# Kernel optimization log

Hardware: AMD Instinct MI355X
Metric: run time of the kernel (lower is better)

The kernel has to match this reference:

```python
import jax, jax.numpy as jnp
import numpy as np

D_IN = 768
D_OUT = 768
NUM_HEADS = 12
HEAD_DIM = D_OUT // NUM_HEADS


def setup_inputs() -> dict:
    key = jax.random.key(0)
    ks = jax.random.split(key, 6)
    s = 0.02
    x = jax.random.normal(ks[0], (2, 4096, D_IN), dtype=jnp.float32)
    w_query = jax.random.normal(ks[1], (D_IN, D_OUT), dtype=jnp.float32) * s
    w_key = jax.random.normal(ks[2], (D_IN, D_OUT), dtype=jnp.float32) * s
    w_value = jax.random.normal(ks[3], (D_IN, D_OUT), dtype=jnp.float32) * s
    w_out = jax.random.normal(ks[4], (D_OUT, D_OUT), dtype=jnp.float32) * s
    b_out = jnp.zeros((D_OUT,), dtype=jnp.float32)
    return {"x": x, "w_query": w_query, "w_key": w_key, "w_value": w_value,
            "w_out": w_out, "b_out": b_out}


def reference(x, w_query, w_key, w_value, w_out, b_out):
    b, n, _ = x.shape
    # projections -> [b, n, h, d]
    q = (x @ w_query).reshape(b, n, NUM_HEADS, HEAD_DIM)
    k = (x @ w_key).reshape(b, n, NUM_HEADS, HEAD_DIM)
    v = (x @ w_value).reshape(b, n, NUM_HEADS, HEAD_DIM)
    # scores [b, h, q, k]
    scores = jnp.einsum('bqhd,bkhd->bhqk', q, k)
    causal = jnp.triu(jnp.ones((n, n), dtype=bool), k=1)  # True above diagonal
    scores = jnp.where(causal, -jnp.inf, scores)
    scale = 1.0 / jnp.sqrt(jnp.asarray(HEAD_DIM, dtype=scores.dtype))
    weights = jax.nn.softmax(scores * scale, axis=-1)
    # dropout p=0.0 -> identity
    ctx = jnp.einsum('bhqk,bkhd->bqhd', weights, v).reshape(b, n, D_OUT)
    return ctx @ w_out + b_out
```

## Files before the change

kernel.cpp:

```cpp
#include <hip/hip_runtime.h>

typedef unsigned short ushort_t;
typedef __bf16 bf16_t;
typedef float floatx4 __attribute__((ext_vector_type(4)));
typedef bf16_t bf16x8 __attribute__((ext_vector_type(8)));
typedef float f32x4 __attribute__((ext_vector_type(4)));
typedef unsigned short u16x4 __attribute__((ext_vector_type(4)));
typedef unsigned int u32x2 __attribute__((ext_vector_type(2)));

#define NTOK 4096
#define NHEAD 12
#define HD 64
#define DMODEL 768
#define NROWS 8192

__device__ __forceinline__ ushort_t f2bf(float f) {
  union { float f; unsigned u; } v; v.f = f;
  unsigned u = v.u;
  unsigned r = u + 0x7fffu + ((u >> 16) & 1u);
  return (ushort_t)(r >> 16);
}

__device__ __forceinline__ void async16(const void* g, void* l) {
  __builtin_amdgcn_global_load_lds(
      (const __attribute__((address_space(1))) void*)g,
      (__attribute__((address_space(3))) void*)l, 16, 0, 0);
}


__global__ __launch_bounds__(256) void transpose_w4(
    const float* __restrict__ s0, const float* __restrict__ s1,
    const float* __restrict__ s2, const float* __restrict__ s3,
    ushort_t* __restrict__ d_qkv, ushort_t* __restrict__ d_o) {
  __shared__ float t[32][33];
  const int m = blockIdx.z;
  const float* src = (m == 0) ? s0 : (m == 1) ? s1 : (m == 2) ? s2 : s3;
  ushort_t* dst = (m < 3) ? (d_qkv + (size_t)m * DMODEL * DMODEL) : d_o;
  const int bi = blockIdx.x, bj = blockIdx.y;
  const int r = threadIdx.x >> 5, c = threadIdx.x & 31;
  for (int p = 0; p < 4; ++p)
    t[r + p * 8][c] = src[(size_t)(bi * 32 + r + p * 8) * DMODEL + bj * 32 + c];
  __syncthreads();
  for (int p = 0; p < 4; ++p)
    dst[(size_t)(bj * 32 + r + p * 8) * DMODEL + bi * 32 + c] = f2bf(t[c][r + p * 8]);
}

__global__ void convert_x(const float* __restrict__ in, ushort_t* __restrict__ out) {
  int idx = blockIdx.x * 256 + threadIdx.x;
  f32x4 v = ((const f32x4*)in)[idx];
  u16x4 o;
  o.x = f2bf(v.x); o.y = f2bf(v.y); o.z = f2bf(v.z); o.w = f2bf(v.w);
  ((u16x4*)out)[idx] = o;
}

__global__ __launch_bounds__(256) void gemm_bt(
    const ushort_t* __restrict__ A, const ushort_t* __restrict__ B, int K, int mode,
    ushort_t* __restrict__ q_ws, ushort_t* __restrict__ k_ws, ushort_t* __restrict__ v_ws,
    float* __restrict__ outF, const float* __restrict__ bias) {
  __shared__ __align__(16) ushort_t a_lds[128 * 32];
  __shared__ __align__(16) ushort_t b_lds[128 * 32];
  const int tid = threadIdx.x;
  const int w = tid >> 6, lane = tid & 63;
  const int quad = lane >> 4, l16 = lane & 15;
  const int wm = w >> 1, wn = w & 1;
  const size_t row0 = (size_t)blockIdx.x * 128;
  const size_t col0 = (size_t)blockIdx.y * 128;

  const int srow = w * 32 + (lane >> 2);
  const int kbyte = (lane & 3) * 16;
  const char* aG = (const char*)(A + (row0 + srow) * (size_t)K) + kbyte;
  const char* bG = (const char*)(B + (col0 + srow) * (size_t)K) + kbyte;
  const size_t rstep = (size_t)16 * K * 2;
  char* aL = (char*)a_lds + (size_t)(w * 2) * 1024;
  char* bL = (char*)b_lds + (size_t)(w * 2) * 1024;

  floatx4 acc[4][4];
  for (int i = 0; i < 4; ++i)
    for (int j = 0; j < 4; ++j) acc[i][j] = (floatx4){0.f, 0.f, 0.f, 0.f};

  const int nk = K / 32;
  for (int kt = 0; kt < nk; ++kt) {
    const size_t koff = (size_t)kt * 64;
    __syncthreads();
    async16(aG + koff, aL);
    async16(aG + koff + rstep, aL + 1024);
    async16(bG + koff, bL);
    async16(bG + koff + rstep, bL + 1024);
    __syncthreads();
    bf16x8 af[4], bfr[4];
    for (int mt = 0; mt < 4; ++mt)
      af[mt] = *(bf16x8*)&a_lds[(wm * 64 + mt * 16 + l16) * 32 + quad * 8];
    for (int nt = 0; nt < 4; ++nt)
      bfr[nt] = *(bf16x8*)&b_lds[(wn * 64 + nt * 16 + l16) * 32 + quad * 8];
    for (int mt = 0; mt < 4; ++mt)
      for (int nt = 0; nt < 4; ++nt)
        acc[mt][nt] = __builtin_amdgcn_mfma_f32_16x16x32_bf16(af[mt], bfr[nt], acc[mt][nt], 0, 0, 0);
  }

  if (mode == 0) {
    const int which = (int)(col0 / DMODEL);
    if (which < 2) {
      ushort_t* dstT = (which == 0) ? q_ws : k_ws;
      const float scale = (which == 0) ? 0.125f : 1.0f;
      for (int mt = 0; mt < 4; ++mt) {
        int gr = (int)row0 + wm * 64 + mt * 16 + quad * 4;
        int b = gr >> 12;
        int n0 = gr & 4095;
        for (int nt = 0; nt < 4; ++nt) {
          int gc = (int)col0 + wn * 64 + nt * 16 + l16;
          int cc = gc - which * DMODEL;
          int h = cc >> 6, d = cc & 63;
          size_t base = ((size_t)(b * NHEAD + h) * NTOK + n0) * HD + d;
          for (int r = 0; r < 4; ++r)
            dstT[base + (size_t)r * HD] = f2bf(acc[mt][nt][r] * scale);
        }
      }
    } else {
      for (int mt = 0; mt < 4; ++mt) {
        int gr = (int)row0 + wm * 64 + mt * 16 + quad * 4;
        int b = gr >> 12;
        int n0 = gr & 4095;
        for (int nt = 0; nt < 4; ++nt) {
          int gc = (int)col0 + wn * 64 + nt * 16 + l16;
          int cc = gc - 2 * DMODEL;
          int h = cc >> 6, d = cc & 63;
          u16x4 ov;
          for (int r = 0; r < 4; ++r) ov[r] = f2bf(acc[mt][nt][r]);
          *(u16x4*)&v_ws[((size_t)(b * NHEAD + h) * HD + d) * NTOK + n0] = ov;
        }
      }
    }
  } else {
    for (int mt = 0; mt < 4; ++mt) {
      int gr = (int)row0 + wm * 64 + mt * 16 + quad * 4;
      for (int nt = 0; nt < 4; ++nt) {
        int gc = (int)col0 + wn * 64 + nt * 16 + l16;
        float bv = bias[gc];
        for (int r = 0; r < 4; ++r)
          outF[(size_t)(gr + r) * DMODEL + gc] = acc[mt][nt][r] + bv;
      }
    }
  }
}

__global__ __launch_bounds__(128) void attn4(
    const ushort_t* __restrict__ Qh, const ushort_t* __restrict__ Kh,
    const ushort_t* __restrict__ Vt, ushort_t* __restrict__ ctx) {
  __shared__ __align__(16) ushort_t k_lds[2][8 * 512];
  __shared__ __align__(16) ushort_t v_lds[2][8 * 512];
  __shared__ __align__(16) ushort_t q_lds[8 * 512];
  const int tid = threadIdx.x;
  const int w = tid >> 6, lane = tid & 63;
  const int quad = lane >> 4, l16 = lane & 15;
  const int bh = blockIdx.x;
  const int b = bh / NHEAD, h = bh % NHEAD;
  const size_t hbase = (size_t)bh * NTOK * HD;
  const ushort_t* Qb = Qh + hbase;
  const ushort_t* Kb = Kh + hbase;
  const ushort_t* Vb = Vt + hbase;

  for (int phase = 0; phase < 2; ++phase) {
    const int qt = (phase == 0) ? (int)blockIdx.y : 63 - (int)blockIdx.y;
    const int Q0 = qt * 64;
    const int nkt = qt + 1;
    __syncthreads();
#pragma unroll
    for (int i = 0; i < 4; ++i) {
      int s = w * 4 + i;
      async16(Qb + (size_t)(Q0 + (s >> 1) * 16 + l16) * HD + (s & 1) * 32 + quad * 8,
              (char*)q_lds + s * 1024);
    }
#pragma unroll
    for (int i = 0; i < 4; ++i) {
      int s = w * 4 + i;
      async16(Kb + (size_t)((s >> 1) * 16 + l16) * HD + (s & 1) * 32 + quad * 8,
              (char*)k_lds + s * 1024);
      async16(Vb + (size_t)((s >> 1) * 16 + l16) * NTOK + (s & 1) * 32 + quad * 8,
              (char*)v_lds + s * 1024);
    }
    __asm volatile("s_waitcnt vmcnt(0)" ::: "memory");
    bf16x8 qr[2][2];
#pragma unroll
    for (int qf = 0; qf < 2; ++qf)
#pragma unroll
      for (int hh = 0; hh < 2; ++hh)
        qr[qf][hh] = *(const bf16x8*)((const char*)q_lds + (((w * 2 + qf) * 2 + hh) * 1024) + lane * 16);

    floatx4 o[2][4];
    float lp[2] = {0.f, 0.f};
#pragma unroll
    for (int qf = 0; qf < 2; ++qf)
#pragma unroll
      for (int dt = 0; dt < 4; ++dt) o[qf][dt] = (floatx4){0.f, 0.f, 0.f, 0.f};

    const int wq0 = Q0 + w * 32;

    for (int kt = 0; kt < nkt; ++kt) {
      const int cur = kt & 1;
      __syncthreads();
      if (kt + 1 < nkt) {
        const int k1 = (kt + 1) * 64;
#pragma unroll
        for (int i = 0; i < 4; ++i) {
          int s = w * 4 + i;
          async16(Kb + (size_t)(k1 + (s >> 1) * 16 + l16) * HD + (s & 1) * 32 + quad * 8,
                  (char*)k_lds + (cur ^ 1) * 8192 + s * 1024);
          async16(Vb + (size_t)((s >> 1) * 16 + l16) * NTOK + k1 + (s & 1) * 32 + quad * 8,
                  (char*)v_lds + (cur ^ 1) * 8192 + s * 1024);
        }
      }
      const char* kb = (const char*)k_lds + cur * 8192;
      const char* vb = (const char*)v_lds + cur * 8192;

      floatx4 st[2][4];
#pragma unroll
      for (int mt = 0; mt < 4; ++mt) {
        bf16x8 kf0 = *(const bf16x8*)(kb + (mt * 2 + 0) * 1024 + lane * 16);
        bf16x8 kf1 = *(const bf16x8*)(kb + (mt * 2 + 1) * 1024 + lane * 16);
#pragma unroll
        for (int qf = 0; qf < 2; ++qf) {
          floatx4 z = (floatx4){0.f, 0.f, 0.f, 0.f};
          z = __builtin_amdgcn_mfma_f32_16x16x32_bf16(kf0, qr[qf][0], z, 0, 0, 0);
          z = __builtin_amdgcn_mfma_f32_16x16x32_bf16(kf1, qr[qf][1], z, 0, 0, 0);
          st[qf][mt] = z;
        }
      }
      const int k0 = kt * 64;
      const bool need_mask = (kt == nkt - 1);
#pragma unroll
      for (int qf = 0; qf < 2; ++qf) {
        const int qg = wq0 + qf * 16 + l16;
        float sum = 0.f;
#pragma unroll
        for (int mt = 0; mt < 4; ++mt) {
          float p[4];
#pragma unroll
          for (int r = 0; r < 4; ++r) {
            float e = __expf(st[qf][mt][r]);
            if (need_mask && (k0 + mt * 16 + quad * 4 + r > qg)) e = 0.f;
            p[r] = e;
            sum += e;
          }
          union { float f; unsigned u; } c0, c1, c2, c3;
          c0.f = p[0]; c1.f = p[1]; c2.f = p[2]; c3.f = p[3];
          u32x2 pk;
          pk.x = (c0.u >> 16) | (c1.u & 0xffff0000u);
          pk.y = (c2.u >> 16) | (c3.u & 0xffff0000u);
          char* dst = (char*)q_lds + (((w * 2 + qf) * 2 + (mt >> 1)) * 1024)
                      + ((((mt & 1) * 2 + (quad >> 1)) * 16 + l16) * 16) + (quad & 1) * 8;
          *(u32x2*)dst = pk;
        }
        lp[qf] += sum;
      }
      __asm volatile("s_waitcnt lgkmcnt(0)" ::: "memory");
      bf16x8 pf[2][2];
#pragma unroll
      for (int qf = 0; qf < 2; ++qf)
#pragma unroll
        for (int hh = 0; hh < 2; ++hh)
          pf[qf][hh] = *(const bf16x8*)((const char*)q_lds + (((w * 2 + qf) * 2 + hh) * 1024) + lane * 16);
#pragma unroll
      for (int dt = 0; dt < 4; ++dt) {
        bf16x8 vf0 = *(const bf16x8*)(vb + (dt * 2 + 0) * 1024 + lane * 16);
        bf16x8 vf1 = *(const bf16x8*)(vb + (dt * 2 + 1) * 1024 + lane * 16);
#pragma unroll
        for (int qf = 0; qf < 2; ++qf) {
          o[qf][dt] = __builtin_amdgcn_mfma_f32_16x16x32_bf16(pf[qf][0], vf0, o[qf][dt], 0, 0, 0);
          o[qf][dt] = __builtin_amdgcn_mfma_f32_16x16x32_bf16(pf[qf][1], vf1, o[qf][dt], 0, 0, 0);
        }
      }
    }

#pragma unroll
    for (int qf = 0; qf < 2; ++qf) {
      float lf = lp[qf];
      lf += __shfl_xor(lf, 16);
      lf += __shfl_xor(lf, 32);
#pragma unroll
      for (int r = 0; r < 4; ++r) {
        float lq = __shfl(lf, quad * 4 + r);
        float inv = 1.0f / lq;
        int qg = wq0 + qf * 16 + quad * 4 + r;
        size_t base = ((size_t)b * NTOK + qg) * DMODEL + h * HD;
#pragma unroll
        for (int dt = 0; dt < 4; ++dt)
          ctx[base + dt * 16 + l16] = f2bf(o[qf][dt][r] * inv);
      }
    }
  }
}

extern "C" void kernel_launch(void* const* d_in, const int* in_sizes, int n_in,
                              void* d_out, int out_size, void* d_ws, size_t ws_size,
                              hipStream_t stream) {
  const float* x  = (const float*)d_in[0];
  const float* wq = (const float*)d_in[1];
  const float* wk = (const float*)d_in[2];
  const float* wv = (const float*)d_in[3];
  const float* wo = (const float*)d_in[4];
  const float* bo = (const float*)d_in[5];
  float* out = (float*)d_out;

  ushort_t* ws = (ushort_t*)d_ws;
  ushort_t* wqkvT = ws;
  ushort_t* woutT = wqkvT + 2304 * 768;
  ushort_t* xbf   = woutT + 768 * 768;
  ushort_t* qh    = xbf + (size_t)NROWS * DMODEL;
  ushort_t* kh    = qh + (size_t)24 * NTOK * HD;
  ushort_t* vt    = kh + (size_t)24 * NTOK * HD;

  transpose_w4<<<dim3(24, 24, 4), 256, 0, stream>>>(wq, wk, wv, wo, wqkvT, woutT);
  convert_x<<<6144, 256, 0, stream>>>(x, xbf);

  gemm_bt<<<dim3(64, 18), 256, 0, stream>>>(xbf, wqkvT, DMODEL, 0,
                                            qh, kh, vt, nullptr, nullptr);
  attn4<<<dim3(24, 32), 128, 0, stream>>>(qh, kh, vt, xbf );
  gemm_bt<<<dim3(64, 6), 256, 0, stream>>>(xbf, woutT, DMODEL, 1,
                                           nullptr, nullptr, nullptr, out, bo);
}
```

Before: 282.5 us.

## Split attention KV range across two blocks and combine partials

Attention now uses 256-thread blocks covering 128 query rows, and the key range of each query tile is split across two blocks (grid z=2). Each block writes unnormalized bf16 partial outputs plus row sums, and a new combine kernel adds them and normalizes into the context buffer. The exponent uses exp2 with log2(e) folded into the Q scale, and the bf16 packing uses a byte-permute instruction. This aims to raise parallelism and balance causal work. In exchange it adds a kernel launch, extra global traffic for the partials, and a second bf16 rounding step. The unstabilized softmax (no max subtraction) is kept unchanged.

Result: no change. 282.6 us (+0.0%).

```diff
diff --git a/kernel.cpp b/kernel.cpp
--- a/kernel.cpp
+++ b/kernel.cpp
@@ -13,12 +13,17 @@
 #define HD 64
 #define DMODEL 768
 #define NROWS 8192
+#define NBH 24
 
 __device__ __forceinline__ ushort_t f2bf(float f) {
   union { float f; unsigned u; } v; v.f = f;
   unsigned u = v.u;
   unsigned r = u + 0x7fffu + ((u >> 16) & 1u);
   return (ushort_t)(r >> 16);
+}
+
+__device__ __forceinline__ float bf2f(ushort_t s) {
+  union { unsigned u; float f; } v; v.u = (unsigned)s << 16; return v.f;
 }
 
 __device__ __forceinline__ void async16(const void* g, void* l) {
@@ -101,7 +106,7 @@
     const int which = (int)(col0 / DMODEL);
     if (which < 2) {
       ushort_t* dstT = (which == 0) ? q_ws : k_ws;
-      const float scale = (which == 0) ? 0.125f : 1.0f;
+      const float scale = (which == 0) ? 0.125f * 1.4426950408889634f : 1.0f;
       for (int mt = 0; mt < 4; ++mt) {
         int gr = (int)row0 + wm * 64 + mt * 16 + quad * 4;
         int b = gr >> 12;
@@ -143,26 +148,32 @@
   }
 }
 
-__global__ __launch_bounds__(128) void attn4(
+__global__ __launch_bounds__(256) void attn5(
     const ushort_t* __restrict__ Qh, const ushort_t* __restrict__ Kh,
-    const ushort_t* __restrict__ Vt, ushort_t* __restrict__ ctx) {
+    const ushort_t* __restrict__ Vt, ushort_t* __restrict__ o_part,
+    float* __restrict__ l_part) {
   __shared__ __align__(16) ushort_t k_lds[2][8 * 512];
   __shared__ __align__(16) ushort_t v_lds[2][8 * 512];
-  __shared__ __align__(16) ushort_t q_lds[8 * 512];
+  __shared__ __align__(16) ushort_t q_lds[16 * 512];
   const int tid = threadIdx.x;
   const int w = tid >> 6, lane = tid & 63;
   const int quad = lane >> 4, l16 = lane & 15;
   const int bh = blockIdx.x;
-  const int b = bh / NHEAD, h = bh % NHEAD;
+  const int split = blockIdx.z;
   const size_t hbase = (size_t)bh * NTOK * HD;
   const ushort_t* Qb = Qh + hbase;
   const ushort_t* Kb = Kh + hbase;
   const ushort_t* Vb = Vt + hbase;
+  const size_t obase = ((size_t)split * NBH + bh) * NTOK * HD;
+  const size_t lbase = ((size_t)split * NBH + bh) * NTOK;
 
   for (int phase = 0; phase < 2; ++phase) {
-    const int qt = (phase == 0) ? (int)blockIdx.y : 63 - (int)blockIdx.y;
-    const int Q0 = qt * 64;
-    const int nkt = qt + 1;
+    const int qt = (phase == 0) ? (int)blockIdx.y : 31 - (int)blockIdx.y;
+    const int Q0 = qt * 128;
+    const int nkt = 2 * qt + 2;
+    const int kt_lo = (split == 0) ? 0 : nkt / 2;
+    const int kt_hi = (split == 0) ? nkt / 2 : nkt;
+    const int nit = kt_hi - kt_lo;
     __syncthreads();
 #pragma unroll
     for (int i = 0; i < 4; ++i) {
@@ -170,13 +181,16 @@
       async16(Qb + (size_t)(Q0 + (s >> 1) * 16 + l16) * HD + (s & 1) * 32 + quad * 8,
               (char*)q_lds + s * 1024);
     }
-#pragma unroll
-    for (int i = 0; i < 4; ++i) {
-      int s = w * 4 + i;
-      async16(Kb + (size_t)((s >> 1) * 16 + l16) * HD + (s & 1) * 32 + quad * 8,
-              (char*)k_lds + s * 1024);
-      async16(Vb + (size_t)((s >> 1) * 16 + l16) * NTOK + (s & 1) * 32 + quad * 8,
-              (char*)v_lds + s * 1024);
+    {
+      const int k0p = kt_lo * 64;
+#pragma unroll
+      for (int i = 0; i < 2; ++i) {
+        int s = w * 2 + i;
+        async16(Kb + (size_t)(k0p + (s >> 1) * 16 + l16) * HD + (s & 1) * 32 + quad * 8,
+                (char*)k_lds + s * 1024);
+        async16(Vb + (size_t)((s >> 1) * 16 + l16) * NTOK + k0p + (s & 1) * 32 + quad * 8,
+                (char*)v_lds + s * 1024);
+      }
     }
     __asm volatile("s_waitcnt vmcnt(0)" ::: "memory");
     bf16x8 qr[2][2];
@@ -184,7 +198,7 @@
     for (int qf = 0; qf < 2; ++qf)
 #pragma unroll
       for (int hh = 0; hh < 2; ++hh)
-        qr[qf][hh] = *(const bf16x8*)((const char*)q_lds + (((w * 2 + qf) * 2 + hh) * 1024) + lane * 16);
+        qr[qf][hh] = *(const bf16x8*)((const char*)q_lds + ((w * 4 + qf * 2 + hh) * 1024) + lane * 16);
 
     floatx4 o[2][4];
     float lp[2] = {0.f, 0.f};
@@ -195,20 +209,23 @@
 
     const int wq0 = Q0 + w * 32;
 
-    for (int kt = 0; kt < nkt; ++kt) {
-      const int cur = kt & 1;
+    for (int it = 0; it < nit; ++it) {
+      const int kt = kt_lo + it;
+      const int cur = it & 1;
       __syncthreads();
-      if (kt + 1 < nkt) {
+      if (it + 1 < nit) {
         const int k1 = (kt + 1) * 64;
 #pragma unroll
-        for (int i = 0; i < 4; ++i) {
-          int s = w * 4 + i;
+        for (int i = 0; i < 2; ++i) {
+          int s = w * 2 + i;
           async16(Kb + (size_t)(k1 + (s >> 1) * 16 + l16) * HD + (s & 1) * 32 + quad * 8,
                   (char*)k_lds + (cur ^ 1) * 8192 + s * 1024);
           async16(Vb + (size_t)((s >> 1) * 16 + l16) * NTOK + k1 + (s & 1) * 32 + quad * 8,
                   (char*)v_lds + (cur ^ 1) * 8192 + s * 1024);
         }
       }
+      const int k0 = kt * 64;
+      if (k0 > wq0 + 31) continue;
       const char* kb = (const char*)k_lds + cur * 8192;
       const char* vb = (const char*)v_lds + cur * 8192;
 
@@ -225,8 +242,7 @@
           st[qf][mt] = z;
         }
       }
-      const int k0 = kt * 64;
-      const bool need_mask = (kt == nkt - 1);
+      const bool need_mask = (k0 + 63 > wq0);
 #pragma unroll
       for (int qf = 0; qf < 2; ++qf) {
         const int qg = wq0 + qf * 16 + l16;
@@ -236,7 +252,7 @@
           float p[4];
 #pragma unroll
           for (int r = 0; r < 4; ++r) {
-            float e = __expf(st[qf][mt][r]);
+            float e = __builtin_exp2f(st[qf][mt][r]);
             if (need_mask && (k0 + mt * 16 + quad * 4 + r > qg)) e = 0.f;
             p[r] = e;
             sum += e;
@@ -244,9 +260,9 @@
           union { float f; unsigned u; } c0, c1, c2, c3;
           c0.f = p[0]; c1.f = p[1]; c2.f = p[2]; c3.f = p[3];
           u32x2 pk;
-          pk.x = (c0.u >> 16) | (c1.u & 0xffff0000u);
-          pk.y = (c2.u >> 16) | (c3.u & 0xffff0000u);
-          char* dst = (char*)q_lds + (((w * 2 + qf) * 2 + (mt >> 1)) * 1024)
+          pk.x = __builtin_amdgcn_perm(c1.u, c0.u, 0x07060302u);
+          pk.y = __builtin_amdgcn_perm(c3.u, c2.u, 0x07060302u);
+          char* dst = (char*)q_lds + ((w * 4 + qf * 2 + (mt >> 1)) * 1024)
                       + ((((mt & 1) * 2 + (quad >> 1)) * 16 + l16) * 16) + (quad & 1) * 8;
           *(u32x2*)dst = pk;
         }
@@ -258,7 +274,7 @@
       for (int qf = 0; qf < 2; ++qf)
 #pragma unroll
         for (int hh = 0; hh < 2; ++hh)
-          pf[qf][hh] = *(const bf16x8*)((const char*)q_lds + (((w * 2 + qf) * 2 + hh) * 1024) + lane * 16);
+          pf[qf][hh] = *(const bf16x8*)((const char*)q_lds + ((w * 4 + qf * 2 + hh) * 1024) + lane * 16);
 #pragma unroll
       for (int dt = 0; dt < 4; ++dt) {
         bf16x8 vf0 = *(const bf16x8*)(vb + (dt * 2 + 0) * 1024 + lane * 16);
@@ -279,15 +295,33 @@
 #pragma unroll
       for (int r = 0; r < 4; ++r) {
         float lq = __shfl(lf, quad * 4 + r);
-        float inv = 1.0f / lq;
         int qg = wq0 + qf * 16 + quad * 4 + r;
-        size_t base = ((size_t)b * NTOK + qg) * DMODEL + h * HD;
+        size_t base = obase + (size_t)qg * HD;
 #pragma unroll
         for (int dt = 0; dt < 4; ++dt)
-          ctx[base + dt * 16 + l16] = f2bf(o[qf][dt][r] * inv);
+          o_part[base + dt * 16 + l16] = f2bf(o[qf][dt][r]);
+        if (l16 == 0) l_part[lbase + qg] = lq;
       }
     }
   }
+}
+
+__global__ __launch_bounds__(256) void combine(
+    const ushort_t* __restrict__ o_part, const float* __restrict__ l_part,
+    ushort_t* __restrict__ ctx) {
+  const int row = blockIdx.x * 16 + (threadIdx.x >> 4);
+  const int d = (threadIdx.x & 15) * 4;
+  const int bh = row >> 12, n = row & 4095;
+  const int b = bh / NHEAD, h = bh % NHEAD;
+  const size_t i0 = (size_t)row * HD + d;
+  const size_t i1 = i0 + (size_t)NBH * NTOK * HD;
+  u16x4 a = *(const u16x4*)&o_part[i0];
+  u16x4 c = *(const u16x4*)&o_part[i1];
+  float inv = 1.0f / (l_part[row] + l_part[row + NBH * NTOK]);
+  u16x4 ov;
+#pragma unroll
+  for (int j = 0; j < 4; ++j) ov[j] = f2bf((bf2f(a[j]) + bf2f(c[j])) * inv);
+  *(u16x4*)&ctx[((size_t)b * NTOK + n) * DMODEL + h * HD + d] = ov;
 }
 
 extern "C" void kernel_launch(void* const* d_in, const int* in_sizes, int n_in,
@@ -306,15 +340,18 @@
   ushort_t* woutT = wqkvT + 2304 * 768;
   ushort_t* xbf   = woutT + 768 * 768;
   ushort_t* qh    = xbf + (size_t)NROWS * DMODEL;
-  ushort_t* kh    = qh + (size_t)24 * NTOK * HD;
-  ushort_t* vt    = kh + (size_t)24 * NTOK * HD;
+  ushort_t* kh    = qh + (size_t)NBH * NTOK * HD;
+  ushort_t* vt    = kh + (size_t)NBH * NTOK * HD;
+  ushort_t* opart = vt + (size_t)NBH * NTOK * HD;
+  float*    lpart = (float*)(opart + (size_t)2 * NBH * NTOK * HD);
 
   transpose_w4<<<dim3(24, 24, 4), 256, 0, stream>>>(wq, wk, wv, wo, wqkvT, woutT);
   convert_x<<<6144, 256, 0, stream>>>(x, xbf);
 
   gemm_bt<<<dim3(64, 18), 256, 0, stream>>>(xbf, wqkvT, DMODEL, 0,
                                             qh, kh, vt, nullptr, nullptr);
-  attn4<<<dim3(24, 32), 128, 0, stream>>>(qh, kh, vt, xbf );
+  attn5<<<dim3(24, 16, 2), 256, 0, stream>>>(qh, kh, vt, opart, lpart);
+  combine<<<(NBH * NTOK) / 16, 256, 0, stream>>>(opart, lpart, xbf );
   gemm_bt<<<dim3(64, 6), 256, 0, stream>>>(xbf, woutT, DMODEL, 1,
                                            nullptr, nullptr, nullptr, out, bo);
 }
```
